# Kernel tuning notes

Hardware: AMD Instinct MI355X
Metric: run time of the kernel (lower is better)

The kernel has to match this reference:

```python
import jax, jax.numpy as jnp
import numpy as np

N_NODES = 100000
N_EDGES = 3200000
M = 24
HID = 32
OUT = 16


def neighbor_mean(feat, row, col, num_nodes):
    # sum features of source nodes into destination nodes, divide by in-degree
    sums = jax.ops.segment_sum(feat[row], col, num_segments=num_nodes)  # (N, F)
    deg = jax.ops.segment_sum(jnp.ones_like(col, dtype=feat.dtype), col, num_segments=num_nodes)
    return sums / jnp.clip(deg, 1.0)[:, None]


def sage_conv(x, row, col, num_nodes, w_l, b_l, w_r):
    # PyG SAGEConv(aggr='mean'): lin_l(mean_aggr) + lin_r(x); lin_r has no bias
    aggr = neighbor_mean(x, row, col, num_nodes)
    return aggr @ w_l.T + b_l + x @ w_r.T


def setup_inputs() -> dict:
    key = jax.random.key(0)
    ks = jax.random.split(key, 10)
    x_bin = jax.random.randint(ks[0], (N_NODES, M), 0, 2).astype(jnp.float32)
    edge_index = jax.random.randint(ks[1], (2, N_EDGES), 0, N_NODES).astype(jnp.int64)
    s = 0.1
    return {
        "x_bin": x_bin,
        "edge_index": edge_index,
        "w1l": s * jax.random.normal(ks[2], (HID, M), jnp.float32),
        "b1": s * jax.random.normal(ks[3], (HID,), jnp.float32),
        "w1r": s * jax.random.normal(ks[4], (HID, M), jnp.float32),
        "w2l": s * jax.random.normal(ks[5], (OUT, HID), jnp.float32),
        "b2": s * jax.random.normal(ks[6], (OUT,), jnp.float32),
        "w2r": s * jax.random.normal(ks[7], (OUT, HID), jnp.float32),
        "head_w": s * jax.random.normal(ks[8], (1, 3 * M + OUT), jnp.float32),
        "head_b": s * jax.random.normal(ks[9], (1,), jnp.float32),
    }


def reference(x_bin, edge_index, w1l, b1, w1r, w2l, b2, w2r, head_w, head_b):
    num_nodes = x_bin.shape[0]
    row, col = edge_index[0], edge_index[1]
    # explicit branch: [self markers | neighbor fraction | self * neighbor fraction]
    frac1 = neighbor_mean(x_bin, row, col, num_nodes)
    feats = jnp.concatenate([x_bin, frac1, x_bin * frac1], axis=1)  # (N, 3M)
    # GNN branch: SmallSAGE (dropout is identity at inference)
    h = jax.nn.relu(sage_conv(x_bin, row, col, num_nodes, w1l, b1, w1r))
    emb = jax.nn.relu(sage_conv(h, row, col, num_nodes, w2l, b2, w2r))  # (N, OUT)
    z = jnp.concatenate([feats, emb], axis=1)  # (N, 3M+OUT)
    yhat = (z @ head_w.T + head_b)[:, 0]  # (N,)
    return yhat, z
```

## Files before the change

### kernel.cpp

```cpp
#include <hip/hip_runtime.h>
#include <hip/hip_bf16.h>

#define MF 24
#define HIDF 32
#define OUTF 16
#define ZDIM 88
#define NPB 8
#define NPB2 32
#define SW1 28
#define SW2 36

#define NB 512
#define EB 4096
#define CAP 8192


union bf16x8 {
    float4 v;
    __hip_bfloat16 h[8];
};
union bf16x2u {
    unsigned int u;
    __hip_bfloat16 h[2];
};

__device__ __forceinline__ float ldw(const void* p, size_t i, bool bf16) {
    return bf16 ? __bfloat162float(((const __hip_bfloat16*)p)[i])
                : ((const float*)p)[i];
}

__device__ __forceinline__ bool detect_bf(const unsigned int* __restrict__ xw) {
    unsigned int w = xw[threadIdx.x & 63];
    return __ballot((w & 0xFFFFu) == 0x3F80u) != 0ull;
}
__device__ __forceinline__ bool detect_i64(const unsigned int* __restrict__ ew) {
    unsigned int w = ew[2 * (threadIdx.x & 63) + 1];
    return __popcll(__ballot(w == 0u)) >= 32;
}

__device__ __forceinline__ int bkt_of(int c, unsigned long long Wm) {
    return (int)(((unsigned long long)(unsigned)c * Wm) >> 32);
}

__device__ __forceinline__ float bf_lo(unsigned u) { return __uint_as_float(u << 16); }
__device__ __forceinline__ float bf_hi(unsigned u) { return __uint_as_float(u & 0xFFFF0000u); }

#define HIST_EDGE(c_)                                                   \
    if ((unsigned)(c_) < (unsigned)N) atomicAdd(&hist[bkt_of(c_, Wm)], 1);

__global__ __launch_bounds__(256) void k_histA(
    const void* __restrict__ x, unsigned int* __restrict__ xpack,
    const int* __restrict__ ei, int* __restrict__ counts,
    int nE, int N, unsigned long long Wm) {
    const bool bf16 = detect_bf((const unsigned int*)x);
    const bool i64 = detect_i64((const unsigned int*)ei);

    for (int n = blockIdx.x * 256 + threadIdx.x; n < N; n += gridDim.x * 256) {
        unsigned int m = 0;
        if (bf16) {
            const float4* xr = reinterpret_cast<const float4*>(
                (const __hip_bfloat16*)x + (size_t)n * MF);
            bf16x8 u;
#pragma unroll
            for (int q = 0; q < 3; ++q) {
                u.v = xr[q];
#pragma unroll
                for (int i = 0; i < 8; ++i)
                    if (__bfloat162float(u.h[i]) != 0.f) m |= 1u << (q * 8 + i);
            }
        } else {
            const float* xr = (const float*)x + (size_t)n * MF;
#pragma unroll
            for (int k = 0; k < MF; ++k)
                if (xr[k] != 0.f) m |= 1u << k;
        }
        xpack[n] = m;
    }

    __shared__ int hist[NB];
    for (int i = threadIdx.x; i < NB; i += 256) hist[i] = 0;
    __syncthreads();
    size_t base = (size_t)blockIdx.x * EB;
    int m = nE - (int)base;
    if (m > EB) m = EB;
    if (!(nE & 1)) {
        int nPair = m >> 1;
        if (i64) {
            const int4* cp = (const int4*)ei + (((size_t)nE + base) >> 1);
            for (int j = threadIdx.x; j < nPair; j += 256) {
                int4 c4 = cp[j];
                HIST_EDGE(c4.x);
                HIST_EDGE(c4.z);
            }
        } else {
            const int2* cp = (const int2*)ei + (((size_t)nE + base) >> 1);
            for (int j = threadIdx.x; j < nPair; j += 256) {
                int2 c2 = cp[j];
                HIST_EDGE(c2.x);
                HIST_EDGE(c2.y);
            }
        }
        for (int i = (nPair << 1) + threadIdx.x; i < m; i += 256) {
            size_t e = base + i;
            int c = i64 ? ei[2 * ((size_t)nE + e)] : ei[(size_t)nE + e];
            HIST_EDGE(c);
        }
    } else {
        for (int i = threadIdx.x; i < m; i += 256) {
            size_t e = base + i;
            int c = i64 ? ei[2 * ((size_t)nE + e)] : ei[(size_t)nE + e];
            HIST_EDGE(c);
        }
    }
    __syncthreads();
    for (int i = threadIdx.x; i < NB; i += 256)
        counts[(size_t)blockIdx.x * NB + i] = hist[i];
}

__global__ __launch_bounds__(1024) void k_colscan(int* __restrict__ counts,
                                                  int* __restrict__ colSum, int nBlk) {
    __shared__ int s[1024];
    int b = blockIdx.x, t = threadIdx.x;
    int v = (t < nBlk) ? counts[(size_t)t * NB + b] : 0;
    s[t] = v;
    __syncthreads();
    for (int off = 1; off < 1024; off <<= 1) {
        int y = (t >= off) ? s[t - off] : 0;
        __syncthreads();
        s[t] += y;
        __syncthreads();
    }
    if (t < nBlk) counts[(size_t)t * NB + b] = s[t] - v;
    if (t == 1023) colSum[b] = s[1023];
}

#define SCAT_EDGE(r_, c_)                                               \
    if ((unsigned)(c_) < (unsigned)N) {                                 \
        int b_ = bkt_of(c_, Wm);                                        \
        int ld_ = (c_) - b_ * W;                                        \
        unsigned rr_ = ((unsigned)(r_) < (unsigned)N) ? (unsigned)(r_) : 0u; \
        int pos_ = ldsStart[b_] + atomicAdd(&lcnt[b_], 1);              \
        rec[pos_] = rr_ | ((unsigned)ld_ << 20);                        \
        bkt[pos_] = (unsigned short)b_;                                 \
    }

__global__ __launch_bounds__(256) void k_scatB(
    const int* __restrict__ ei, const int* __restrict__ counts,
    const int* __restrict__ colSum,
    unsigned int* __restrict__ part, int nE, int N, int W,
    unsigned long long Wm, int nBlk) {
    const bool i64 = detect_i64((const unsigned int*)ei);
    __shared__ unsigned int rec[EB];
    __shared__ unsigned short bkt[EB];
    __shared__ int ldsStart[NB + 1];
    __shared__ int lcnt[NB];
    __shared__ int base2[NB];
    __shared__ int s256[256];
    const int t = threadIdx.x, blk = blockIdx.x;

    {
        int a0 = colSum[2 * t], a1 = colSum[2 * t + 1];
        int ps = a0 + a1;
        s256[t] = ps;
        __syncthreads();
        for (int off = 1; off < 256; off <<= 1) {
            int y = (t >= off) ? s256[t - off] : 0;
            __syncthreads();
            s256[t] += y;
            __syncthreads();
        }
        int base = s256[t] - ps;
        ldsStart[2 * t] = base;
        ldsStart[2 * t + 1] = base + a0;
        __syncthreads();
    }
    for (int b = t; b < NB; b += 256) {
        base2[b] = ldsStart[b] + counts[(size_t)blk * NB + b];
        lcnt[b] = 0;
    }
    __syncthreads();

    {
        int p0 = counts[(size_t)blk * NB + 2 * t];
        int p1 = counts[(size_t)blk * NB + 2 * t + 1];
        int n0 = (blk + 1 < nBlk) ? counts[(size_t)(blk + 1) * NB + 2 * t] : colSum[2 * t];
        int n1 = (blk + 1 < nBlk) ? counts[(size_t)(blk + 1) * NB + 2 * t + 1] : colSum[2 * t + 1];
        int v0 = n0 - p0, v1 = n1 - p1;
        int ps = v0 + v1;
        s256[t] = ps;
        __syncthreads();
        for (int off = 1; off < 256; off <<= 1) {
            int y = (t >= off) ? s256[t - off] : 0;
            __syncthreads();
            s256[t] += y;
            __syncthreads();
        }
        int base = s256[t] - ps;
        ldsStart[2 * t] = base;
        ldsStart[2 * t + 1] = base + v0;
        if (t == 255) ldsStart[NB] = base + ps;
        __syncthreads();
    }
    for (int b = t; b < NB; b += 256) base2[b] -= ldsStart[b];
    __syncthreads();

    size_t eb = (size_t)blk * EB;
    int m = nE - (int)eb;
    if (m > EB) m = EB;
    if (!(nE & 1)) {
        int nPair = m >> 1;
        if (i64) {
            const int4* rp = (const int4*)ei + (eb >> 1);
            const int4* cp = (const int4*)ei + (((size_t)nE + eb) >> 1);
            for (int j = t; j < nPair; j += 256) {
                int4 r4 = rp[j];
                int4 c4 = cp[j];
                SCAT_EDGE(r4.x, c4.x);
                SCAT_EDGE(r4.z, c4.z);
            }
        } else {
            const int2* rp = (const int2*)ei + (eb >> 1);
            const int2* cp = (const int2*)ei + (((size_t)nE + eb) >> 1);
            for (int j = t; j < nPair; j += 256) {
                int2 r2 = rp[j];
                int2 c2 = cp[j];
                SCAT_EDGE(r2.x, c2.x);
                SCAT_EDGE(r2.y, c2.y);
            }
        }
        for (int i = (nPair << 1) + t; i < m; i += 256) {
            size_t e = eb + i;
            int r = i64 ? ei[2 * e] : ei[e];
            int c = i64 ? ei[2 * ((size_t)nE + e)] : ei[(size_t)nE + e];
            SCAT_EDGE(r, c);
        }
    } else {
        for (int i = t; i < m; i += 256) {
            size_t e = eb + i;
            int r = i64 ? ei[2 * e] : ei[e];
            int c = i64 ? ei[2 * ((size_t)nE + e)] : ei[(size_t)nE + e];
            SCAT_EDGE(r, c);
        }
    }
    __syncthreads();

    int total = ldsStart[NB];
    for (int i = t; i < total; i += 256) {
        int b = bkt[i];
        part[base2[b] + i] = rec[i];
    }
}

__global__ __launch_bounds__(256) void k_csrC(const int* __restrict__ colSum,
                                              unsigned int* __restrict__ part,
                                              int* __restrict__ degi,
                                              int* __restrict__ rowstart,
                                              const unsigned int* __restrict__ xpack,
                                              unsigned int* __restrict__ cnt3,
                                              int N, int W) {
    __shared__ unsigned int stage[CAP];
    __shared__ unsigned long long c3[256 * 3];
    __shared__ int hist[256];
    __shared__ int sc[256];
    __shared__ int cur[256];
    int b = blockIdx.x, t = threadIdx.x;

    int p = ((t < b) ? colSum[t] : 0) + ((t + 256 < b) ? colSum[t + 256] : 0);
    sc[t] = p;
    hist[t] = 0;
#pragma unroll
    for (int j = 0; j < 3; ++j) c3[t * 3 + j] = 0ull;
    __syncthreads();
    for (int off = 128; off > 0; off >>= 1) {
        if (t < off) sc[t] += sc[t + off];
        __syncthreads();
    }
    int start = sc[0];
    int bs = colSum[b];
    int node = b * W + t;

    __syncthreads();

    if (bs > CAP) {
        if (t < W && node < N) {
            degi[node] = 0; rowstart[node] = start;
#pragma unroll
            for (int j = 0; j < 6; ++j) cnt3[(size_t)node * 6 + j] = 0;
        }
        return;
    }

    for (int i = t; i < bs; i += 256) {
        unsigned int v = part[start + i];
        stage[i] = v;
        int ld = v >> 20;
        atomicAdd(&hist[ld], 1);
        unsigned int xp = xpack[v & 0xFFFFFu];
        int b3 = ld * 3;
#pragma unroll
        for (int j = 0; j < 3; ++j) {
            unsigned int nlo = (xp >> (8 * j)) & 0xFu;
            unsigned int nhi = (xp >> (8 * j + 4)) & 0xFu;
            unsigned long long inc =
                (unsigned long long)((nlo * 0x00204081u) & 0x01010101u) |
                ((unsigned long long)((nhi * 0x00204081u) & 0x01010101u) << 32);
            atomicAdd(&c3[b3 + j], inc);
        }
    }
    __syncthreads();

    int v = hist[t];
    sc[t] = v;
    __syncthreads();
    for (int off = 1; off < 256; off <<= 1) {
        int y = (t >= off) ? sc[t - off] : 0;
        __syncthreads();
        sc[t] += y;
        __syncthreads();
    }
    int excl = sc[t] - v;
    if (t < W && node < N) {
        degi[node] = v;
        rowstart[node] = start + excl;
        const unsigned int* c3w = (const unsigned int*)c3;
#pragma unroll
        for (int j = 0; j < 6; ++j) cnt3[(size_t)node * 6 + j] = c3w[t * 6 + j];
    }
    cur[t] = excl;
    __syncthreads();

    for (int i = t; i < bs; i += 256) {
        unsigned int v2 = stage[i];
        int pos = atomicAdd(&cur[v2 >> 20], 1);
        part[start + pos] = v2 & 0xFFFFFu;
    }
}

__global__ __launch_bounds__(256) void k_layer1(
    const void* __restrict__ x, const unsigned int* __restrict__ xpack,
    const int* __restrict__ degi, const unsigned int* __restrict__ cnt3,
    void* __restrict__ out,
    const void* __restrict__ w1l, const void* __restrict__ b1,
    const void* __restrict__ w1r, const void* __restrict__ w2l,
    const void* __restrict__ b2, const void* __restrict__ w2r,
    const void* __restrict__ head_w,
    __hip_bfloat16* __restrict__ hl, __hip_bfloat16* __restrict__ st,
    float* __restrict__ ypart, int N) {
    const bool bf16 = detect_bf((const unsigned int*)x);
    __shared__ float swl[HIDF * SW1];
    __shared__ float swr[HIDF * SW1];
    __shared__ float sb[HIDF];
    __shared__ float s2l[OUTF * SW2];
    __shared__ float s2r[OUTF * SW2];
    __shared__ float sb2[OUTF];
    __shared__ float shw[3 * MF];
    __shared__ float fs[NPB][MF];
    __shared__ float hs[NPB][HIDF];
    const int t = threadIdx.x;

    if (bf16) {
        const uint4* al = (const uint4*)w1l;
        const uint4* ar = (const uint4*)w1r;
        if (t < 96) {
            uint4 vl = al[t], vr = ar[t];
            int i0 = t * 8;
            int j = i0 / MF, k = i0 - j * MF;
            float4 fl0 = make_float4(bf_lo(vl.x), bf_hi(vl.x), bf_lo(vl.y), bf_hi(vl.y));
            float4 fl1 = make_float4(bf_lo(vl.z), bf_hi(vl.z), bf_lo(vl.w), bf_hi(vl.w));
            float4 fr0 = make_float4(bf_lo(vr.x), bf_hi(vr.x), bf_lo(vr.y), bf_hi(vr.y));
            float4 fr1 = make_float4(bf_lo(vr.z), bf_hi(vr.z), bf_lo(vr.w), bf_hi(vr.w));
            float4* dl = (float4*)(swl + j * SW1 + k);
            float4* dr = (float4*)(swr + j * SW1 + k);
            dl[0] = fl0; dl[1] = fl1;
            dr[0] = fr0; dr[1] = fr1;
        }
        const uint4* bl = (const uint4*)w2l;
        const uint4* br = (const uint4*)w2r;
        if (t >= 128 && t < 192) {
            int c = t - 128;
            uint4 vl = bl[c], vr = br[c];
            int i0 = c * 8;
            int o = i0 >> 5, j = i0 & 31;
            float4 fl0 = make_float4(bf_lo(vl.x), bf_hi(vl.x), bf_lo(vl.y), bf_hi(vl.y));
            float4 fl1 = make_float4(bf_lo(vl.z), bf_hi(vl.z), bf_lo(vl.w), bf_hi(vl.w));
            float4 fr0 = make_float4(bf_lo(vr.x), bf_hi(vr.x), bf_lo(vr.y), bf_hi(vr.y));
            float4 fr1 = make_float4(bf_lo(vr.z), bf_hi(vr.z), bf_lo(vr.w), bf_hi(vr.w));
            float4* dl = (float4*)(s2l + o * SW2 + j);
            float4* dr = (float4*)(s2r + o * SW2 + j);
            dl[0] = fl0; dl[1] = fl1;
            dr[0] = fr0; dr[1] = fr1;
        }
    } else {
        const float4* al = (const float4*)w1l;
        const float4* ar = (const float4*)w1r;
        if (t < 192) {
            float4 vl = al[t], vr = ar[t];
            int i0 = t * 4;
            int j = i0 / MF, k = i0 - j * MF;
            *(float4*)(swl + j * SW1 + k) = vl;
            *(float4*)(swr + j * SW1 + k) = vr;
        }
        const float4* bl = (const float4*)w2l;
        const float4* br = (const float4*)w2r;
        int c = t - 128;
        if (c >= 0 && c < 128) {
            float4 vl = bl[c], vr = br[c];
            int i0 = c * 4;
            int o = i0 >> 5, j = i0 & 31;
            *(float4*)(s2l + o * SW2 + j) = vl;
            *(float4*)(s2r + o * SW2 + j) = vr;
        }
    }
    if (t < HIDF) sb[t] = ldw(b1, t, bf16);
    if (t >= 64 && t < 64 + OUTF) sb2[t - 64] = ldw(b2, t - 64, bf16);
    if (t >= 96 && t < 96 + 3 * MF) shw[t - 96] = ldw(head_w, t - 96, bf16);
    __syncthreads();

    const int lane = threadIdx.x & 31;
    const int wg = threadIdx.x >> 5;
    int node = blockIdx.x * NPB + wg;
    bool valid = node < N;

    int dg = 0;
    unsigned int xpn = 0;
    unsigned int cw = 0;
    if (valid) {
        dg = degi[node];
        xpn = xpack[node];
        if (lane < MF) cw = cnt3[(size_t)node * 6 + (lane >> 2)];
    }
    int cnt = (cw >> ((lane & 3) * 8)) & 0xFF;

    float inv = 1.f / fmaxf((float)dg, 1.f);
    float fv = (float)cnt * inv;
    float xv = (float)((xpn >> lane) & 1);

    float pc = 0.f;
    if (valid && lane < MF) {
        if (bf16) {
            __hip_bfloat16* z = (__hip_bfloat16*)out + N + (size_t)node * ZDIM;
            z[lane] = __float2bfloat16(xv);
            z[MF + lane] = __float2bfloat16(fv);
            z[2 * MF + lane] = __float2bfloat16(xv * fv);
        } else {
            float* z = (float*)out + N + (size_t)node * ZDIM;
            z[lane] = xv;
            z[MF + lane] = fv;
            z[2 * MF + lane] = xv * fv;
        }
        pc = xv * shw[lane] + fv * shw[MF + lane] + xv * fv * shw[2 * MF + lane];
    }

    if (lane < MF) fs[wg][lane] = fv;

    float fvk[MF];
    {
        const float4* fp = (const float4*)fs[wg];
#pragma unroll
        for (int q = 0; q < 6; ++q) {
            float4 f4 = fp[q];
            fvk[q * 4 + 0] = f4.x; fvk[q * 4 + 1] = f4.y;
            fvk[q * 4 + 2] = f4.z; fvk[q * 4 + 3] = f4.w;
        }
    }
    float wlv[MF], wrv[MF];
    {
        const float4* wl4 = (const float4*)(swl + lane * SW1);
        const float4* wr4 = (const float4*)(swr + lane * SW1);
#pragma unroll
        for (int q = 0; q < 6; ++q) {
            float4 a = wl4[q], b = wr4[q];
            wlv[q * 4 + 0] = a.x; wlv[q * 4 + 1] = a.y;
            wlv[q * 4 + 2] = a.z; wlv[q * 4 + 3] = a.w;
            wrv[q * 4 + 0] = b.x; wrv[q * 4 + 1] = b.y;
            wrv[q * 4 + 2] = b.z; wrv[q * 4 + 3] = b.w;
        }
    }
    float acc = sb[lane];
#pragma unroll
    for (int k = 0; k < MF; ++k) {
        acc = fmaf(fvk[k], wlv[k], acc);
        acc += ((xpn >> k) & 1u) ? wrv[k] : 0.f;
    }
    hs[wg][lane] = fmaxf(acc, 0.f);

#pragma unroll
    for (int off = 16; off > 0; off >>= 1) pc += __shfl_down(pc, off, 32);

    int o = lane & 15;
    int half = lane >> 4;
    const float4* wrow4 = (const float4*)((half ? s2r : s2l) + o * SW2);
    const float4* hp4 = (const float4*)hs[wg];
    float d = 0.f;
#pragma unroll
    for (int q = 0; q < 8; ++q) {
        float4 hq = hp4[q], wq = wrow4[q];
        d += hq.x * wq.x + hq.y * wq.y + hq.z * wq.z + hq.w * wq.w;
    }
    if (valid) {
        if (half == 0) hl[(size_t)node * OUTF + o] = __float2bfloat16(d);
        else st[(size_t)node * OUTF + o] = __float2bfloat16(d + sb2[o]);
        if (lane == 0) ypart[node] = pc;
    }
}

__global__ __launch_bounds__(256) void k_layer2(
    const void* __restrict__ x, const int* __restrict__ degi,
    const int* __restrict__ rowstart, const unsigned int* __restrict__ srcs,
    const __hip_bfloat16* __restrict__ hl, const __hip_bfloat16* __restrict__ st,
    const float* __restrict__ ypart, void* __restrict__ out,
    const void* __restrict__ head_w, const void* __restrict__ head_b, int N) {
    const bool bf16 = detect_bf((const unsigned int*)x);
    __shared__ float shw2[OUTF];
    __shared__ float shb;
    if (threadIdx.x < OUTF) shw2[threadIdx.x] = ldw(head_w, 3 * MF + threadIdx.x, bf16);
    if (threadIdx.x == 0) shb = ldw(head_b, 0, bf16);
    __syncthreads();

    int lane = threadIdx.x & 7;
    int g = threadIdx.x >> 3;
    int node = blockIdx.x * NPB2 + g;
    bool valid = node < N;

    int dg = 0, p0 = 0;
    if (valid) {
        dg = degi[node];
        p0 = rowstart[node];
    }
    const unsigned int* hlw = (const unsigned int*)hl;
    float s0 = 0.f, s1 = 0.f;
    int e = 0;
    for (; e + 8 <= dg; e += 8) {
        int i0 = srcs[p0 + e],     i1 = srcs[p0 + e + 1];
        int i2 = srcs[p0 + e + 2], i3 = srcs[p0 + e + 3];
        int i4 = srcs[p0 + e + 4], i5 = srcs[p0 + e + 5];
        int i6 = srcs[p0 + e + 6], i7 = srcs[p0 + e + 7];
        bf16x2u u0, u1, u2, u3, u4, u5, u6, u7;
        u0.u = hlw[(size_t)i0 * 8 + lane];
        u1.u = hlw[(size_t)i1 * 8 + lane];
        u2.u = hlw[(size_t)i2 * 8 + lane];
        u3.u = hlw[(size_t)i3 * 8 + lane];
        u4.u = hlw[(size_t)i4 * 8 + lane];
        u5.u = hlw[(size_t)i5 * 8 + lane];
        u6.u = hlw[(size_t)i6 * 8 + lane];
        u7.u = hlw[(size_t)i7 * 8 + lane];
        s0 += (__bfloat162float(u0.h[0]) + __bfloat162float(u1.h[0])) +
              (__bfloat162float(u2.h[0]) + __bfloat162float(u3.h[0])) +
              (__bfloat162float(u4.h[0]) + __bfloat162float(u5.h[0])) +
              (__bfloat162float(u6.h[0]) + __bfloat162float(u7.h[0]));
        s1 += (__bfloat162float(u0.h[1]) + __bfloat162float(u1.h[1])) +
              (__bfloat162float(u2.h[1]) + __bfloat162float(u3.h[1])) +
              (__bfloat162float(u4.h[1]) + __bfloat162float(u5.h[1])) +
              (__bfloat162float(u6.h[1]) + __bfloat162float(u7.h[1]));
    }
    for (; e + 4 <= dg; e += 4) {
        int a = srcs[p0 + e], b = srcs[p0 + e + 1];
        int c = srcs[p0 + e + 2], d = srcs[p0 + e + 3];
        bf16x2u ua, ub, uc, ud;
        ua.u = hlw[(size_t)a * 8 + lane];
        ub.u = hlw[(size_t)b * 8 + lane];
        uc.u = hlw[(size_t)c * 8 + lane];
        ud.u = hlw[(size_t)d * 8 + lane];
        s0 += (__bfloat162float(ua.h[0]) + __bfloat162float(ub.h[0])) +
              (__bfloat162float(uc.h[0]) + __bfloat162float(ud.h[0]));
        s1 += (__bfloat162float(ua.h[1]) + __bfloat162float(ub.h[1])) +
              (__bfloat162float(uc.h[1]) + __bfloat162float(ud.h[1]));
    }
    for (; e < dg; ++e) {
        bf16x2u ua;
        ua.u = hlw[(size_t)srcs[p0 + e] * 8 + lane];
        s0 += __bfloat162float(ua.h[0]);
        s1 += __bfloat162float(ua.h[1]);
    }

    float emb0 = 0.f, emb1 = 0.f;
    if (valid) {
        float inv = 1.f / fmaxf((float)dg, 1.f);
        bf16x2u us;
        us.u = ((const unsigned int*)st)[(size_t)node * 8 + lane];
        emb0 = fmaxf(s0 * inv + __bfloat162float(us.h[0]), 0.f);
        emb1 = fmaxf(s1 * inv + __bfloat162float(us.h[1]), 0.f);
        if (bf16) {
            bf16x2u up;
            up.h[0] = __float2bfloat16(emb0);
            up.h[1] = __float2bfloat16(emb1);
            unsigned int* zw = (unsigned int*)((__hip_bfloat16*)out + N +
                                               (size_t)node * ZDIM + 3 * MF);
            zw[lane] = up.u;
        } else {
            float2* zw = (float2*)((float*)out + N + (size_t)node * ZDIM + 3 * MF);
            zw[lane] = make_float2(emb0, emb1);
        }
    }
    float part = emb0 * shw2[2 * lane] + emb1 * shw2[2 * lane + 1];
#pragma unroll
    for (int off = 4; off > 0; off >>= 1) part += __shfl_down(part, off, 8);
    if (valid && lane == 0) {
        float y = ypart[node] + part + shb;
        if (bf16) ((__hip_bfloat16*)out)[node] = __float2bfloat16(y);
        else ((float*)out)[node] = y;
    }
}

extern "C" void kernel_launch(void* const* d_in, const int* in_sizes, int n_in,
                              void* d_out, int out_size, void* d_ws, size_t ws_size,
                              hipStream_t stream) {
    const void* x = d_in[0];
    const int* ei = (const int*)d_in[1];
    const void* w1l = d_in[2];
    const void* b1 = d_in[3];
    const void* w1r = d_in[4];
    const void* w2l = d_in[5];
    const void* b2 = d_in[6];
    const void* w2r = d_in[7];
    const void* head_w = d_in[8];
    const void* head_b = d_in[9];

    const int N = in_sizes[0] / MF;
    const int nE = in_sizes[1] / 2;
    const int W = (N + NB - 1) / NB;
    const unsigned long long Wm = (0x100000000ull / (unsigned)W) + 1;
    const int nBlkA = (nE + EB - 1) / EB;

    if (N > NB * 256 || N > 131072 || nBlkA > 1024 ||
        (size_t)nBlkA * NB < (size_t)N || nE < 64) return;

    int* colSum = (int*)((char*)d_ws + 256);
    int* degi = colSum + NB;
    int* rowstart = degi + N;
    int* counts = rowstart + N;
    unsigned int* part = (unsigned int*)(counts + (size_t)nBlkA * NB);
    unsigned int* xpack = part + nE;
    __hip_bfloat16* hl = (__hip_bfloat16*)(xpack + N);
    __hip_bfloat16* st = hl + (size_t)N * OUTF;
    unsigned int* cnt3 = (unsigned int*)(st + (size_t)N * OUTF);
    float* ypart = (float*)counts;

    const size_t need = 256 +
        ((size_t)NB + 2 * (size_t)N + (size_t)nBlkA * NB +
         (size_t)nE + (size_t)N + 6 * (size_t)N) * 4 + (size_t)N * OUTF * 2 * 2;
    if (ws_size < need) return;

    const int gb1 = (N + NPB - 1) / NPB;
    const int gb2 = (N + NPB2 - 1) / NPB2;
    k_histA<<<nBlkA, 256, 0, stream>>>(x, xpack, ei, counts, nE, N, Wm);
    k_colscan<<<NB, 1024, 0, stream>>>(counts, colSum, nBlkA);
    k_scatB<<<nBlkA, 256, 0, stream>>>(ei, counts, colSum,
                                       part, nE, N, W, Wm, nBlkA);
    k_csrC<<<NB, 256, 0, stream>>>(colSum, part, degi, rowstart,
                                   xpack, cnt3, N, W);
    k_layer1<<<gb1, 256, 0, stream>>>(x, xpack, degi, cnt3, d_out,
                                      w1l, b1, w1r, w2l, b2, w2r, head_w,
                                      hl, st, ypart, N);
    k_layer2<<<gb2, 256, 0, stream>>>(x, degi, rowstart, part, hl, st, ypart,
                                      d_out, head_w, head_b, N);
}
```

Before: 217.7 us.

## Replace column-scan kernel with atomic bucket totals and atomic cursors

Drops the separate k_colscan kernel. Bucket totals are now accumulated with global atomics at the end of histogram blocks, and each scatter block claims its offset within a bucket through an atomic cursor instead of a precomputed exclusive prefix. This removes one kernel launch and a pass over the counts matrix, at the cost of a memset plus global atomic contention on 512 counters. Edge order within a bucket becomes nondeterministic across blocks, which changes the floating-point summation order downstream.

```diff
diff --git a/kernel.cpp b/kernel.cpp
--- a/kernel.cpp
+++ b/kernel.cpp
@@ -51,7 +51,7 @@
 __global__ __launch_bounds__(256) void k_histA(
     const void* __restrict__ x, unsigned int* __restrict__ xpack,
     const int* __restrict__ ei, int* __restrict__ counts,
-    int nE, int N, unsigned long long Wm) {
+    int* __restrict__ colSum, int nE, int N, unsigned long long Wm) {
     const bool bf16 = detect_bf((const unsigned int*)x);
     const bool i64 = detect_i64((const unsigned int*)ei);
 
@@ -113,25 +113,11 @@
         }
     }
     __syncthreads();
-    for (int i = threadIdx.x; i < NB; i += 256)
-        counts[(size_t)blockIdx.x * NB + i] = hist[i];
-}
-
-__global__ __launch_bounds__(1024) void k_colscan(int* __restrict__ counts,
-                                                  int* __restrict__ colSum, int nBlk) {
-    __shared__ int s[1024];
-    int b = blockIdx.x, t = threadIdx.x;
-    int v = (t < nBlk) ? counts[(size_t)t * NB + b] : 0;
-    s[t] = v;
-    __syncthreads();
-    for (int off = 1; off < 1024; off <<= 1) {
-        int y = (t >= off) ? s[t - off] : 0;
-        __syncthreads();
-        s[t] += y;
-        __syncthreads();
-    }
-    if (t < nBlk) counts[(size_t)t * NB + b] = s[t] - v;
-    if (t == 1023) colSum[b] = s[1023];
+    for (int i = threadIdx.x; i < NB; i += 256) {
+        int h = hist[i];
+        counts[(size_t)blockIdx.x * NB + i] = h;
+        if (h) atomicAdd(&colSum[i], h);
+    }
 }
 
 #define SCAT_EDGE(r_, c_)                                               \
@@ -146,9 +132,9 @@
 
 __global__ __launch_bounds__(256) void k_scatB(
     const int* __restrict__ ei, const int* __restrict__ counts,
-    const int* __restrict__ colSum,
+    const int* __restrict__ colSum, int* __restrict__ gcursor,
     unsigned int* __restrict__ part, int nE, int N, int W,
-    unsigned long long Wm, int nBlk) {
+    unsigned long long Wm) {
     const bool i64 = detect_i64((const unsigned int*)ei);
     __shared__ unsigned int rec[EB];
     __shared__ unsigned short bkt[EB];
@@ -175,17 +161,16 @@
         __syncthreads();
     }
     for (int b = t; b < NB; b += 256) {
-        base2[b] = ldsStart[b] + counts[(size_t)blk * NB + b];
+        int lc = counts[(size_t)blk * NB + b];
         lcnt[b] = 0;
+        int rel = lc ? atomicAdd(&gcursor[b], lc) : 0;
+        base2[b] = ldsStart[b] + rel;
     }
     __syncthreads();
 
     {
-        int p0 = counts[(size_t)blk * NB + 2 * t];
-        int p1 = counts[(size_t)blk * NB + 2 * t + 1];
-        int n0 = (blk + 1 < nBlk) ? counts[(size_t)(blk + 1) * NB + 2 * t] : colSum[2 * t];
-        int n1 = (blk + 1 < nBlk) ? counts[(size_t)(blk + 1) * NB + 2 * t + 1] : colSum[2 * t + 1];
-        int v0 = n0 - p0, v1 = n1 - p1;
+        int v0 = counts[(size_t)blk * NB + 2 * t];
+        int v1 = counts[(size_t)blk * NB + 2 * t + 1];
         int ps = v0 + v1;
         s256[t] = ps;
         __syncthreads();
@@ -626,7 +611,8 @@
         (size_t)nBlkA * NB < (size_t)N || nE < 64) return;
 
     int* colSum = (int*)((char*)d_ws + 256);
-    int* degi = colSum + NB;
+    int* gcursor = colSum + NB;
+    int* degi = gcursor + NB;
     int* rowstart = degi + N;
     int* counts = rowstart + N;
     unsigned int* part = (unsigned int*)(counts + (size_t)nBlkA * NB);
@@ -637,16 +623,16 @@
     float* ypart = (float*)counts;
 
     const size_t need = 256 +
-        ((size_t)NB + 2 * (size_t)N + (size_t)nBlkA * NB +
+        (2 * (size_t)NB + 2 * (size_t)N + (size_t)nBlkA * NB +
          (size_t)nE + (size_t)N + 6 * (size_t)N) * 4 + (size_t)N * OUTF * 2 * 2;
     if (ws_size < need) return;
 
     const int gb1 = (N + NPB - 1) / NPB;
     const int gb2 = (N + NPB2 - 1) / NPB2;
-    k_histA<<<nBlkA, 256, 0, stream>>>(x, xpack, ei, counts, nE, N, Wm);
-    k_colscan<<<NB, 1024, 0, stream>>>(counts, colSum, nBlkA);
-    k_scatB<<<nBlkA, 256, 0, stream>>>(ei, counts, colSum,
-                                       part, nE, N, W, Wm, nBlkA);
+    hipMemsetAsync((void*)colSum, 0, 2 * NB * sizeof(int), stream);
+    k_histA<<<nBlkA, 256, 0, stream>>>(x, xpack, ei, counts, colSum, nE, N, Wm);
+    k_scatB<<<nBlkA, 256, 0, stream>>>(ei, counts, colSum, gcursor,
+                                       part, nE, N, W, Wm);
     k_csrC<<<NB, 256, 0, stream>>>(colSum, part, degi, rowstart,
                                    xpack, cnt3, N, W);
     k_layer1<<<gb1, 256, 0, stream>>>(x, xpack, degi, cnt3, d_out,
```

Result: slower. 246.9 us (+13.4%).
